# Kernel tuning notes

Measured on AMD Instinct MI355X. Metric: run time of the kernel, lower is better.

The kernel has to match this reference:

```python
import jax, jax.numpy as jnp
import numpy as np

B, N, D_IN, D, H_HEADS, DH, M_LAND, ITERS, NCLS = 2, 16384, 1024, 512, 8, 64, 256, 6, 2


def layer_norm(x, g, b, eps=1e-5):
    mu = x.mean(-1, keepdims=True)
    var = ((x - mu) ** 2).mean(-1, keepdims=True)
    return (x - mu) * jax.lax.rsqrt(var + eps) * g + b


def pinv_iter(x, iters):
    # Moore-Penrose pseudo-inverse via Newton-Schulz style iteration (lucidrains nystrom-attention)
    col = jnp.abs(x).sum(-1)
    row = jnp.abs(x).sum(-2)
    z = jnp.swapaxes(x, -1, -2) / (jnp.max(col) * jnp.max(row))
    I = jnp.eye(x.shape[-1], dtype=x.dtype)
    for _ in range(iters):
        xz = x @ z
        z = 0.25 * z @ (13.0 * I - xz @ (15.0 * I - xz @ (7.0 * I - xz)))
    return z


def depthwise_conv(x, w, pad_h, pad_w):
    # x: [B,C,H,W], w: [C,1,kh,kw], groups=C
    return jax.lax.conv_general_dilated(
        x, w, (1, 1), ((pad_h, pad_h), (pad_w, pad_w)),
        dimension_numbers=('NCHW', 'OIHW', 'NCHW'), feature_group_count=x.shape[1])


def nystrom_attention(x, w_qkv, w_out, b_out, res_w):
    b, n, _ = x.shape
    pad = (-n) % M_LAND
    xp = jnp.pad(x, ((0, 0), (pad, 0), (0, 0)))  # pad at front
    npad = n + pad
    qkv = xp @ w_qkv                              # [b, npad, 3D]
    q, k, v = jnp.split(qkv, 3, axis=-1)
    split_heads = lambda t: t.reshape(b, npad, H_HEADS, DH).transpose(0, 2, 1, 3)
    q = split_heads(q) * (DH ** -0.5)
    k = split_heads(k)
    v = split_heads(v)
    l = npad // M_LAND
    # landmarks: mean over contiguous groups '(m l) d -> m d'
    ql = q.reshape(b, H_HEADS, M_LAND, l, DH).mean(3)
    kl = k.reshape(b, H_HEADS, M_LAND, l, DH).mean(3)
    sim1 = jnp.einsum('bhnd,bhmd->bhnm', q, kl)   # [b,h,npad,m]
    sim2 = jnp.einsum('bhid,bhjd->bhij', ql, kl)  # [b,h,m,m]
    sim3 = jnp.einsum('bhmd,bhnd->bhmn', ql, k)   # [b,h,m,npad]
    a1 = jax.nn.softmax(sim1, -1)
    a2 = jax.nn.softmax(sim2, -1)
    a3 = jax.nn.softmax(sim3, -1)
    a2inv = pinv_iter(a2, ITERS)
    out = (a1 @ a2inv) @ (a3 @ v)                 # [b,h,npad,dh]
    # residual depthwise conv over sequence dim, kernel (33,1), per head
    out = out + depthwise_conv(v, res_w, 16, 0)
    out = out.transpose(0, 2, 1, 3).reshape(b, npad, D)
    out = out @ w_out + b_out                     # dropout is identity in eval
    return out[:, -n:]


def ppeg(x, Hs, Ws, w7, b7, w5, b5, w3, b3):
    Bx, _, C = x.shape
    cls_tok, feat = x[:, :1], x[:, 1:]
    f = feat.transpose(0, 2, 1).reshape(Bx, C, Hs, Ws)
    y = (f
         + depthwise_conv(f, w7, 3, 3) + b7[None, :, None, None]
         + depthwise_conv(f, w5, 2, 2) + b5[None, :, None, None]
         + depthwise_conv(f, w3, 1, 1) + b3[None, :, None, None])
    y = y.reshape(Bx, C, Hs * Ws).transpose(0, 2, 1)
    return jnp.concatenate([cls_tok, y], axis=1)


def _forward(x, w_feat, b_feat, cls_token, ln1_g, ln1_b, qkv1, out1_w, out1_b, res1_w,
             ppeg_w7, ppeg_b7, ppeg_w5, ppeg_b5, ppeg_w3, ppeg_b3,
             ln2_g, ln2_b, qkv2, out2_w, out2_b, res2_w, lnf_g, lnf_b, cls_w, cls_b):
    h = jax.nn.gelu(x @ w_feat + b_feat)          # feature embed (dropout off)
    n = h.shape[1]
    side = int(np.ceil(np.sqrt(n)))
    add = side * side - n
    h = jnp.concatenate([h, h[:, :add]], axis=1)  # pad bag to square
    cls = jnp.broadcast_to(cls_token, (h.shape[0], 1, D))
    h = jnp.concatenate([cls, h], axis=1)
    h = h + nystrom_attention(layer_norm(h, ln1_g, ln1_b), qkv1, out1_w, out1_b, res1_w)
    h = ppeg(h, side, side, ppeg_w7, ppeg_b7, ppeg_w5, ppeg_b5, ppeg_w3, ppeg_b3)
    h = h + nystrom_attention(layer_norm(h, ln2_g, ln2_b), qkv2, out2_w, out2_b, res2_w)
    feat0 = layer_norm(h, lnf_g, lnf_b)[:, 0]
    return feat0 @ cls_w + cls_b                  # logits [B, n_classes]


def setup_inputs() -> dict:
    key = jax.random.key(0)
    ks = jax.random.split(key, 16)
    s = jnp.float32(0.02)
    return {
        'x': jax.random.normal(ks[0], (B, N, D_IN), jnp.float32),
        'w_feat': jax.random.normal(ks[1], (D_IN, D), jnp.float32) * s,
        'b_feat': jnp.zeros((D,), jnp.float32),
        'cls_token': jax.random.normal(ks[2], (1, 1, D), jnp.float32) * jnp.float32(1e-6),
        'ln1_g': jnp.ones((D,), jnp.float32), 'ln1_b': jnp.zeros((D,), jnp.float32),
        'qkv1': jax.random.normal(ks[3], (D, 3 * D), jnp.float32) * s,
        'out1_w': jax.random.normal(ks[4], (D, D), jnp.float32) * s,
        'out1_b': jnp.zeros((D,), jnp.float32),
        'res1_w': jax.random.normal(ks[5], (H_HEADS, 1, 33, 1), jnp.float32) * s,
        'ppeg_w7': jax.random.normal(ks[6], (D, 1, 7, 7), jnp.float32) * s,
        'ppeg_b7': jnp.zeros((D,), jnp.float32),
        'ppeg_w5': jax.random.normal(ks[7], (D, 1, 5, 5), jnp.float32) * s,
        'ppeg_b5': jnp.zeros((D,), jnp.float32),
        'ppeg_w3': jax.random.normal(ks[8], (D, 1, 3, 3), jnp.float32) * s,
        'ppeg_b3': jnp.zeros((D,), jnp.float32),
        'ln2_g': jnp.ones((D,), jnp.float32), 'ln2_b': jnp.zeros((D,), jnp.float32),
        'qkv2': jax.random.normal(ks[9], (D, 3 * D), jnp.float32) * s,
        'out2_w': jax.random.normal(ks[10], (D, D), jnp.float32) * s,
        'out2_b': jnp.zeros((D,), jnp.float32),
        'res2_w': jax.random.normal(ks[11], (H_HEADS, 1, 33, 1), jnp.float32) * s,
        'lnf_g': jnp.ones((D,), jnp.float32), 'lnf_b': jnp.zeros((D,), jnp.float32),
        'cls_w': jax.random.normal(ks[12], (D, NCLS), jnp.float32) * s,
        'cls_b': jnp.zeros((NCLS,), jnp.float32),
    }


def reference(x, w_feat, b_feat, cls_token, ln1_g, ln1_b, qkv1, out1_w, out1_b, res1_w,
              ppeg_w7, ppeg_b7, ppeg_w5, ppeg_b5, ppeg_w3, ppeg_b3,
              ln2_g, ln2_b, qkv2, out2_w, out2_b, res2_w, lnf_g, lnf_b, cls_w, cls_b):
    return _forward(x, w_feat, b_feat, cls_token, ln1_g, ln1_b, qkv1, out1_w, out1_b, res1_w,
                    ppeg_w7, ppeg_b7, ppeg_w5, ppeg_b5, ppeg_w3, ppeg_b3,
                    ln2_g, ln2_b, qkv2, out2_w, out2_b, res2_w, lnf_g, lnf_b, cls_w, cls_b)
```

## Files before the change

kernel.cpp:

```cpp
#include <hip/hip_runtime.h>
#include <cstdint>
#include <cstddef>

#define BB 2
#define TT 16385
#define NPAD 16640
#define DD 512
#define HH 8
#define DHH 64
#define MLAND 256
#define PADF 255
#define A3KC 26
#define A3CH 640

typedef __attribute__((ext_vector_type(8))) _Float16 f16x8;
typedef __attribute__((ext_vector_type(4))) float f32x4;

__device__ __forceinline__ float gelu_f(float v) {
  float c = 0.7978845608028654f * (v + 0.044715f * v * v * v);
  return 0.5f * v * (1.0f + tanhf(c));
}

__device__ __forceinline__ unsigned short f16_1(float a) {
  _Float16 h = (_Float16)a;
  return __builtin_bit_cast(unsigned short, h);
}
__device__ __forceinline__ float f16f(unsigned u) {
  return (float)__builtin_bit_cast(_Float16, (unsigned short)(u & 0xffffu));
}
__device__ __forceinline__ unsigned pk_f16(float a, float b) {
  return (unsigned)f16_1(a) | ((unsigned)f16_1(b) << 16);
}
__device__ __forceinline__ void split2h(float a, float b, unsigned& hi, unsigned& lo) {
  _Float16 ah = (_Float16)a, bh = (_Float16)b;
  hi = (unsigned)__builtin_bit_cast(unsigned short, ah) |
       ((unsigned)__builtin_bit_cast(unsigned short, bh) << 16);
  lo = pk_f16(a - (float)ah, b - (float)bh);
}

__device__ __forceinline__ void gload16(const unsigned short* g, short* l) {
  __builtin_amdgcn_global_load_lds(
      (const __attribute__((address_space(1))) void*)g,
      (__attribute__((address_space(3))) void*)l, 16, 0, 0);
}

__global__ void k_set_cls(float* __restrict__ h, const float* __restrict__ cls) {
  h[(size_t)blockIdx.x * TT * DD + threadIdx.x] = cls[threadIdx.x];
}
__global__ void k_copy_cls(float* __restrict__ dst, const float* __restrict__ src) {
  size_t o = (size_t)blockIdx.x * TT * DD + threadIdx.x;
  dst[o] = src[o];
}

__global__ __launch_bounds__(256) void k_cvt_wt(
    const float* __restrict__ W, unsigned short* __restrict__ Wth, int K, int N) {
  __shared__ float tile[32][33];
  int kb = blockIdx.x * 32, nb = blockIdx.y * 32;
  int t = threadIdx.x;
  int tr = t >> 3, tc4 = (t & 7) * 4;
  float4 v = *(const float4*)(W + (size_t)(kb + tr) * N + nb + tc4);
  tile[tr][tc4 + 0] = v.x;
  tile[tr][tc4 + 1] = v.y;
  tile[tr][tc4 + 2] = v.z;
  tile[tr][tc4 + 3] = v.w;
  __syncthreads();
  int n = nb + tr;
  ushort4 hs;
  hs.x = f16_1(tile[tc4 + 0][tr]);
  hs.y = f16_1(tile[tc4 + 1][tr]);
  hs.z = f16_1(tile[tc4 + 2][tr]);
  hs.w = f16_1(tile[tc4 + 3][tr]);
  *(ushort4*)(Wth + (size_t)n * K + kb + tc4) = hs;
}

template <int MODE>
__global__ __launch_bounds__(512) void k_gemm_mfma(
    const float* __restrict__ A, const unsigned short* __restrict__ Aph,
    const unsigned short* __restrict__ Apl, const unsigned short* __restrict__ Wth,
    const float* __restrict__ bias, void* __restrict__ Cv, int M, int K, int N,
    int lda) {
  __shared__ short Ash[128][44];
  __shared__ short Asl[128][44];
  __shared__ short Bsh[256][44];
  const int t = threadIdx.x;
  int nRow = gridDim.x, nCol = gridDim.y;
  int lin = blockIdx.x + blockIdx.y * nRow;
  int chunk = 8 * nCol;
  int group = lin / chunk;
  int rem = lin - group * chunk;
  int gbase = group * 8;
  int Geff = nRow - gbase;
  if (Geff > 8) Geff = 8;
  const int rb = (gbase + rem % Geff) * 128;
  const int cb = (rem / Geff) * 256;
  const float* Ab = A;
  float* Cf = (float*)Cv;
  unsigned short* Ch = (unsigned short*)Cv;
  if (MODE == 2) {
    int b = blockIdx.z;
    Ab = A + (size_t)b * NPAD * DD + (size_t)PADF * DD;
    Cf = (float*)Cv + (size_t)b * TT * DD;
  }
  const int lane = t & 63, wv = t >> 6;
  const int wr = wv >> 2, wc = wv & 3;
  const int fr = lane & 15, kg = lane >> 4;
  const int srow = t >> 2, skh = (t & 3) * 8;
  const int brow = t >> 1, bkh = (t & 1) * 16;

  f32x4 acc[4][4];
  f32x4 zero4 = {0.f, 0.f, 0.f, 0.f};
#pragma unroll
  for (int i = 0; i < 4; ++i)
#pragma unroll
    for (int j = 0; j < 4; ++j) acc[i][j] = zero4;

  for (int k0 = 0; k0 < K; k0 += 32) {
    __syncthreads();
    if (MODE == 1) {
      const unsigned short* ph = Aph + (size_t)(rb + srow) * lda + k0 + skh;
      const unsigned short* pl = Apl + (size_t)(rb + srow) * lda + k0 + skh;
      *(uint4*)&Ash[srow][skh] = *(const uint4*)ph;
      *(uint4*)&Asl[srow][skh] = *(const uint4*)pl;
    } else {
      int grow = rb + srow;
      float4 f0 = {0, 0, 0, 0}, f1 = {0, 0, 0, 0};
      if (grow < M) {
        const float* p = Ab + (size_t)grow * lda + k0 + skh;
        f0 = *(const float4*)p;
        f1 = *(const float4*)(p + 4);
      }
      unsigned h0, h1, h2, h3, l0, l1, l2, l3;
      split2h(f0.x, f0.y, h0, l0);
      split2h(f0.z, f0.w, h1, l1);
      split2h(f1.x, f1.y, h2, l2);
      split2h(f1.z, f1.w, h3, l3);
      *(uint4*)&Ash[srow][skh] = make_uint4(h0, h1, h2, h3);
      *(uint4*)&Asl[srow][skh] = make_uint4(l0, l1, l2, l3);
    }
    {
      const unsigned short* ph = Wth + (size_t)(cb + brow) * K + k0 + bkh;
      *(uint4*)&Bsh[brow][bkh] = *(const uint4*)ph;
      *(uint4*)&Bsh[brow][bkh + 8] = *(const uint4*)(ph + 8);
    }
    __syncthreads();
    f16x8 ah[4], al[4];
#pragma unroll
    for (int mf = 0; mf < 4; ++mf) {
      ah[mf] = *(const f16x8*)&Ash[wr * 64 + mf * 16 + fr][kg * 8];
      al[mf] = *(const f16x8*)&Asl[wr * 64 + mf * 16 + fr][kg * 8];
    }
#pragma unroll
    for (int nf = 0; nf < 4; ++nf) {
      f16x8 bhf = *(const f16x8*)&Bsh[wc * 64 + nf * 16 + fr][kg * 8];
#pragma unroll
      for (int mf = 0; mf < 4; ++mf) {
        acc[mf][nf] =
            __builtin_amdgcn_mfma_f32_16x16x32_f16(ah[mf], bhf, acc[mf][nf], 0, 0, 0);
        acc[mf][nf] =
            __builtin_amdgcn_mfma_f32_16x16x32_f16(al[mf], bhf, acc[mf][nf], 0, 0, 0);
      }
    }
  }
#pragma unroll
  for (int mf = 0; mf < 4; ++mf) {
#pragma unroll
    for (int r = 0; r < 4; ++r) {
      int row = rb + wr * 64 + mf * 16 + kg * 4 + r;
      if (MODE == 2 && row >= M) continue;
      size_t orow = (MODE == 0) ? (size_t)(row + (row >> 14) + 1) : (size_t)row;
#pragma unroll
      for (int nf = 0; nf < 4; ++nf) {
        int col = cb + wc * 64 + nf * 16 + fr;
        float v = acc[mf][nf][r];
        if (MODE == 0) {
          Cf[orow * DD + col] = gelu_f(v + bias[col]);
        } else if (MODE == 1) {
          Ch[orow * (size_t)N + col] = f16_1(v);
        } else {
          float old = Cf[orow * DD + col];
          Cf[orow * DD + col] = old + v + bias[col];
        }
      }
    }
  }
}

__global__ __launch_bounds__(512) void k_gemm_qkv8(
    const unsigned short* __restrict__ Aph, const unsigned short* __restrict__ Wth,
    unsigned short* __restrict__ Ch) {
  __shared__ __align__(16) short Ah[2][128][32];
  __shared__ __align__(16) short Bs[2][256][32];
  const int t = threadIdx.x;
  int nRow = gridDim.x, nCol = gridDim.y;
  int lin = blockIdx.x + blockIdx.y * nRow;
  int chunk = 8 * nCol;
  int group = lin / chunk;
  int rem = lin - group * chunk;
  int gbase = group * 8;
  int Geff = nRow - gbase;
  if (Geff > 8) Geff = 8;
  const int rb = (gbase + rem % Geff) * 128;
  const int cb = (rem / Geff) * 256;
  const int lane = t & 63, wv = t >> 6;
  const int wr = wv >> 2, wc = wv & 3;
  const int fr = lane & 15, kg = lane >> 4;
  const int lr4 = lane >> 2;
  const int ss = (lane & 3) ^ (lr4 & 3);

  f32x4 acc[4][4];
  f32x4 zero4 = {0.f, 0.f, 0.f, 0.f};
#pragma unroll
  for (int i = 0; i < 4; ++i)
#pragma unroll
    for (int j = 0; j < 4; ++j) acc[i][j] = zero4;

  auto STAGE = [&](int kt, int bf) {
    const int k0 = kt * 32;
    {
      int lr = wv * 16;
      gload16(Aph + (size_t)(rb + lr + lr4) * DD + k0 + ss * 8, &Ah[bf][lr][0]);
    }
#pragma unroll
    for (int j = 0; j < 2; ++j) {
      int lr = wv * 32 + j * 16;
      gload16(Wth + (size_t)(cb + lr + lr4) * DD + k0 + ss * 8, &Bs[bf][lr][0]);
    }
  };

  STAGE(0, 0);
  STAGE(1, 1);
  const int sl = ((kg ^ (fr & 3))) * 8;
  for (int kt = 0; kt < 16; ++kt) {
    if (kt < 15) {
      asm volatile("s_waitcnt vmcnt(3)" ::: "memory");
    } else {
      asm volatile("s_waitcnt vmcnt(0)" ::: "memory");
    }
    __builtin_amdgcn_sched_barrier(0);
    __builtin_amdgcn_s_barrier();
    const int bf = kt & 1;
    f16x8 ah[4];
#pragma unroll
    for (int mf = 0; mf < 4; ++mf)
      ah[mf] = *(const f16x8*)&Ah[bf][wr * 64 + mf * 16 + fr][sl];
#pragma unroll
    for (int nf = 0; nf < 4; ++nf) {
      f16x8 bhf = *(const f16x8*)&Bs[bf][wc * 64 + nf * 16 + fr][sl];
#pragma unroll
      for (int mf = 0; mf < 4; ++mf)
        acc[mf][nf] =
            __builtin_amdgcn_mfma_f32_16x16x32_f16(ah[mf], bhf, acc[mf][nf], 0, 0, 0);
    }
    __builtin_amdgcn_s_barrier();
    if (kt + 2 < 16) STAGE(kt + 2, bf);
  }
#pragma unroll
  for (int mf = 0; mf < 4; ++mf) {
#pragma unroll
    for (int r = 0; r < 4; ++r) {
      int row = rb + wr * 64 + mf * 16 + kg * 4 + r;
#pragma unroll
      for (int nf = 0; nf < 4; ++nf) {
        int col = cb + wc * 64 + nf * 16 + fr;
        Ch[(size_t)row * 1536 + col] = f16_1(acc[mf][nf][r]);
      }
    }
  }
}

__global__ __launch_bounds__(512) void k_gemm_proj(
    const unsigned short* __restrict__ Af, const unsigned short* __restrict__ Wth,
    float* __restrict__ Cb, const float* __restrict__ bias) {
  __shared__ __align__(16) short Ah[2][128][32];
  __shared__ __align__(16) short Bs[2][256][32];
  const int t = threadIdx.x;
  int nRow = gridDim.x, nCol = gridDim.y;
  int lin = blockIdx.x + blockIdx.y * nRow;
  int chunk = 8 * nCol;
  int group = lin / chunk;
  int rem = lin - group * chunk;
  int gbase = group * 8;
  int Geff = nRow - gbase;
  if (Geff > 8) Geff = 8;
  const int rb = (gbase + rem % Geff) * 128;
  const int cb = (rem / Geff) * 256;
  const int lane = t & 63, wv = t >> 6;
  const int wr = wv >> 2, wc = wv & 3;
  const int fr = lane & 15, kg = lane >> 4;
  const int lr4 = lane >> 2;
  const int ss = (lane & 3) ^ (lr4 & 3);
  const size_t arow0 = (size_t)blockIdx.z * NPAD + PADF + rb;

  f32x4 acc[4][4];
  f32x4 zero4 = {0.f, 0.f, 0.f, 0.f};
#pragma unroll
  for (int i = 0; i < 4; ++i)
#pragma unroll
    for (int j = 0; j < 4; ++j) acc[i][j] = zero4;

  auto STAGE = [&](int kt, int bf) {
    const int k0 = kt * 32;
    {
      int lr = wv * 16;
      gload16(Af + (arow0 + lr + lr4) * DD + k0 + ss * 8, &Ah[bf][lr][0]);
    }
#pragma unroll
    for (int j = 0; j < 2; ++j) {
      int lr = wv * 32 + j * 16;
      gload16(Wth + (size_t)(cb + lr + lr4) * DD + k0 + ss * 8, &Bs[bf][lr][0]);
    }
  };

  STAGE(0, 0);
  STAGE(1, 1);
  const int sl = ((kg ^ (fr & 3))) * 8;
  for (int kt = 0; kt < 16; ++kt) {
    if (kt < 15) {
      asm volatile("s_waitcnt vmcnt(3)" ::: "memory");
    } else {
      asm volatile("s_waitcnt vmcnt(0)" ::: "memory");
    }
    __builtin_amdgcn_sched_barrier(0);
    __builtin_amdgcn_s_barrier();
    const int bf = kt & 1;
    f16x8 ah[4];
#pragma unroll
    for (int mf = 0; mf < 4; ++mf)
      ah[mf] = *(const f16x8*)&Ah[bf][wr * 64 + mf * 16 + fr][sl];
#pragma unroll
    for (int nf = 0; nf < 4; ++nf) {
      f16x8 bhf = *(const f16x8*)&Bs[bf][wc * 64 + nf * 16 + fr][sl];
#pragma unroll
      for (int mf = 0; mf < 4; ++mf)
        acc[mf][nf] =
            __builtin_amdgcn_mfma_f32_16x16x32_f16(ah[mf], bhf, acc[mf][nf], 0, 0, 0);
    }
    __builtin_amdgcn_s_barrier();
    if (kt + 2 < 16) STAGE(kt + 2, bf);
  }
  float* Cf = Cb + (size_t)blockIdx.z * TT * DD;
#pragma unroll
  for (int mf = 0; mf < 4; ++mf) {
#pragma unroll
    for (int r = 0; r < 4; ++r) {
      int row = rb + wr * 64 + mf * 16 + kg * 4 + r;
      if (row >= TT) continue;
#pragma unroll
      for (int nf = 0; nf < 4; ++nf) {
        int col = cb + wc * 64 + nf * 16 + fr;
        float old = Cf[(size_t)row * DD + col];
        Cf[(size_t)row * DD + col] = old + acc[mf][nf][r] + bias[col];
      }
    }
  }
}

__global__ __launch_bounds__(256) void k_ln_pad(
    unsigned short* __restrict__ xph, const float* __restrict__ h,
    const float* __restrict__ gam, const float* __restrict__ bet) {
  int w = threadIdx.x >> 6, lane = threadIdx.x & 63;
  int row = blockIdx.x * 4 + w;
  if (row >= BB * TT) return;
  int b = row / TT, i = row - b * TT;
  const float* src = h + (size_t)row * DD;
  float4 x0 = *(const float4*)(src + lane * 4);
  float4 x1 = *(const float4*)(src + 256 + lane * 4);
  float s = x0.x + x0.y + x0.z + x0.w + x1.x + x1.y + x1.z + x1.w;
  for (int o = 32; o; o >>= 1) s += __shfl_xor(s, o);
  float mu = s * (1.f / 512.f);
  float q = (x0.x - mu) * (x0.x - mu) + (x0.y - mu) * (x0.y - mu) +
            (x0.z - mu) * (x0.z - mu) + (x0.w - mu) * (x0.w - mu) +
            (x1.x - mu) * (x1.x - mu) + (x1.y - mu) * (x1.y - mu) +
            (x1.z - mu) * (x1.z - mu) + (x1.w - mu) * (x1.w - mu);
  for (int o = 32; o; o >>= 1) q += __shfl_xor(q, o);
  float rs = rsqrtf(q * (1.f / 512.f) + 1e-5f);
  float4 g0 = *(const float4*)(gam + lane * 4);
  float4 g1 = *(const float4*)(gam + 256 + lane * 4);
  float4 b0 = *(const float4*)(bet + lane * 4);
  float4 b1 = *(const float4*)(bet + 256 + lane * 4);
  float4 o0, o1;
  o0.x = (x0.x - mu) * rs * g0.x + b0.x;
  o0.y = (x0.y - mu) * rs * g0.y + b0.y;
  o0.z = (x0.z - mu) * rs * g0.z + b0.z;
  o0.w = (x0.w - mu) * rs * g0.w + b0.w;
  o1.x = (x1.x - mu) * rs * g1.x + b1.x;
  o1.y = (x1.y - mu) * rs * g1.y + b1.y;
  o1.z = (x1.z - mu) * rs * g1.z + b1.z;
  o1.w = (x1.w - mu) * rs * g1.w + b1.w;
  size_t ro = ((size_t)b * NPAD + PADF + i) * DD;
  *(uint2*)(xph + ro + lane * 4) = make_uint2(pk_f16(o0.x, o0.y), pk_f16(o0.z, o0.w));
  *(uint2*)(xph + ro + 256 + lane * 4) =
      make_uint2(pk_f16(o1.x, o1.y), pk_f16(o1.z, o1.w));
}

__global__ void k_zero_pad(unsigned short* __restrict__ xph) {
  int r = blockIdx.x;
  int b = r / PADF, j = r - b * PADF;
  size_t ro = ((size_t)b * NPAD + j) * DD;
  ((unsigned*)(xph + ro))[threadIdx.x] = 0u;
}

__global__ __launch_bounds__(256) void k_landmarks(
    float* __restrict__ ql, float* __restrict__ kl,
    const unsigned short* __restrict__ qkv) {
  int t = threadIdx.x;
  int mi = t >> 6, d = t & 63;
  int blk = blockIdx.x;
  int bh = blk >> 6, mg = blk & 63;
  int b = bh >> 3, h = bh & 7;
  int m = mg * 4 + mi;
  const unsigned short* base = qkv + (size_t)b * NPAD * 1536 + h * 64 + d;
  float sq = 0.f, sk = 0.f;
  int t0 = m * 65;
  for (int j = 0; j < 65; ++j) {
    const unsigned short* p = base + (size_t)(t0 + j) * 1536;
    sq += f16f(p[0]);
    sk += f16f(p[512]);
  }
  ql[((size_t)bh * 256 + m) * 64 + d] = sq * (0.125f / 65.f);
  kl[((size_t)bh * 256 + m) * 64 + d] = sk * (1.f / 65.f);
}

__global__ __launch_bounds__(256) void k_sim2(
    float* __restrict__ sim, const float* __restrict__ ql, const float* __restrict__ kl) {
  __shared__ __align__(16) float Aq[64][68];
  __shared__ __align__(16) float Bk[64][68];
  int t = threadIdx.x;
  int tj = blockIdx.x, ti = blockIdx.y, bh = blockIdx.z;
  int r = t >> 2, cc = (t & 3) * 16;
  const float* ap = ql + ((size_t)bh * 256 + ti * 64 + r) * 64 + cc;
  const float* bp = kl + ((size_t)bh * 256 + tj * 64 + r) * 64 + cc;
#pragma unroll
  for (int i = 0; i < 16; i += 4) {
    *(float4*)&Aq[r][cc + i] = *(const float4*)(ap + i);
    *(float4*)&Bk[r][cc + i] = *(const float4*)(bp + i);
  }
  __syncthreads();
  int tx = t & 15, ty = t >> 4;
  float acc[4][4];
#pragma unroll
  for (int i = 0; i < 4; ++i)
#pragma unroll
    for (int j = 0; j < 4; ++j) acc[i][j] = 0.f;
  for (int d = 0; d < 64; d += 4) {
    float4 a4[4], b4[4];
#pragma unroll
    for (int ii = 0; ii < 4; ++ii) a4[ii] = *(float4*)&Aq[ty * 4 + ii][d];
#pragma unroll
    for (int jj = 0; jj < 4; ++jj) b4[jj] = *(float4*)&Bk[tx * 4 + jj][d];
#pragma unroll
    for (int ii = 0; ii < 4; ++ii)
#pragma unroll
      for (int jj = 0; jj < 4; ++jj)
        acc[ii][jj] += a4[ii].x * b4[jj].x + a4[ii].y * b4[jj].y + a4[ii].z * b4[jj].z +
                       a4[ii].w * b4[jj].w;
  }
#pragma unroll
  for (int ii = 0; ii < 4; ++ii)
#pragma unroll
    for (int jj = 0; jj < 4; ++jj)
      sim[((size_t)bh * 256 + ti * 64 + ty * 4 + ii) * 256 + tj * 64 + tx * 4 + jj] =
          acc[ii][jj];
}

__global__ __launch_bounds__(256) void k_softmax256(float* __restrict__ a) {
  int w = threadIdx.x >> 6, lane = threadIdx.x & 63;
  size_t row = (size_t)blockIdx.x * 4 + w;
  float* p = a + row * 256 + lane * 4;
  float4 v = *(float4*)p;
  float m = fmaxf(fmaxf(v.x, v.y), fmaxf(v.z, v.w));
  for (int o = 32; o; o >>= 1) m = fmaxf(m, __shfl_xor(m, o));
  v.x = expf(v.x - m); v.y = expf(v.y - m);
  v.z = expf(v.z - m); v.w = expf(v.w - m);
  float s = v.x + v.y + v.z + v.w;
  for (int o = 32; o; o >>= 1) s += __shfl_xor(s, o);
  float inv = 1.f / s;
  v.x *= inv; v.y *= inv; v.z *= inv; v.w *= inv;
  *(float4*)p = v;
}

__global__ void k_pinv_sums(float* __restrict__ red, const float* __restrict__ a2) {
  int bh = blockIdx.x, t = threadIdx.x;
  const float* Ab = a2 + (size_t)bh * 65536;
  float s = 0.f;
// ... 419 lines not shown
#pragma unroll
    for (int kw = 0; kw < 2; ++kw) {
      f16x8 vf[4], pf[4];
#pragma unroll
      for (int mf = 0; mf < 4; ++mf)
        vf[mf] = *(const f16x8*)&W2t[mf * 16 + fr][kw * 32 + kg * 8];
#pragma unroll
      for (int nf = 0; nf < 4; ++nf)
        pf[nf] = *(const f16x8*)&Ps[w][nf * 16 + fr][kw * 32 + kg * 8];
#pragma unroll
      for (int mf = 0; mf < 4; ++mf)
#pragma unroll
        for (int nf = 0; nf < 4; ++nf)
          oacc[mf][nf] = __builtin_amdgcn_mfma_f32_16x16x32_f16(vf[mf], pf[nf],
                                                                oacc[mf][nf], 0, 0, 0);
    }
  }
#pragma unroll
  for (int nf = 0; nf < 4; ++nf) {
    Lp[nf] += __shfl_xor(Lp[nf], 16);
    Lp[nf] += __shfl_xor(Lp[nf], 32);
  }
#pragma unroll
  for (int nf = 0; nf < 4; ++nf) {
    float inv = 1.0f / Lp[nf];
    int tok = n0 + w * 64 + nf * 16 + fr;
#pragma unroll
    for (int mf = 0; mf < 4; ++mf) {
      f32x4 o = oacc[mf][nf];
      ushort4 hs;
      hs.x = f16_1(o[0] * inv);
      hs.y = f16_1(o[1] * inv);
      hs.z = f16_1(o[2] * inv);
      hs.w = f16_1(o[3] * inv);
      *(ushort4*)(attf + ((size_t)b * NPAD + tok) * DD + h * 64 + mf * 16 + kg * 4) = hs;
    }
  }
}

__global__ __launch_bounds__(256) void k_convres(
    unsigned short* __restrict__ attf, const unsigned short* __restrict__ qkv,
    const float* __restrict__ resw) {
  __shared__ float vS[96][68];
  __shared__ float w33[33];
  int t = threadIdx.x;
  int tb = blockIdx.x, bh = blockIdx.y;
  int b = bh >> 3, h = bh & 7;
  int n0 = tb * 64;
  if (t < 33) w33[t] = resw[h * 33 + t];
  int sc = (t & 3) * 16;
#pragma unroll
  for (int pass = 0; pass < 2; ++pass) {
    int r = (t >> 2) + pass * 64;
    if (r < 96) {
      int seq = n0 - 16 + r;
      if (seq >= 0 && seq < NPAD) {
        const unsigned short* p =
            qkv + ((size_t)b * NPAD + seq) * 1536 + 1024 + h * 64 + sc;
        uint4 u0 = *(const uint4*)p;
        uint4 u1 = *(const uint4*)(p + 8);
        float4 f0 = make_float4(f16f(u0.x), f16f(u0.x >> 16), f16f(u0.y),
                                f16f(u0.y >> 16));
        float4 f1 = make_float4(f16f(u0.z), f16f(u0.z >> 16), f16f(u0.w),
                                f16f(u0.w >> 16));
        float4 f2 = make_float4(f16f(u1.x), f16f(u1.x >> 16), f16f(u1.y),
                                f16f(u1.y >> 16));
        float4 f3 = make_float4(f16f(u1.z), f16f(u1.z >> 16), f16f(u1.w),
                                f16f(u1.w >> 16));
        *(float4*)&vS[r][sc + 0] = f0;
        *(float4*)&vS[r][sc + 4] = f1;
        *(float4*)&vS[r][sc + 8] = f2;
        *(float4*)&vS[r][sc + 12] = f3;
      } else {
        float4 z = make_float4(0.f, 0.f, 0.f, 0.f);
        *(float4*)&vS[r][sc + 0] = z;
        *(float4*)&vS[r][sc + 4] = z;
        *(float4*)&vS[r][sc + 8] = z;
        *(float4*)&vS[r][sc + 12] = z;
      }
    }
  }
  __syncthreads();
  int tg = t >> 5;
  int d2 = (t & 31) * 2;
  float ax[8], ay[8];
#pragma unroll
  for (int j = 0; j < 8; ++j) { ax[j] = 0.f; ay[j] = 0.f; }
#pragma unroll
  for (int rr = 0; rr < 40; ++rr) {
    float2 v = *(float2*)&vS[tg * 8 + rr][d2];
#pragma unroll
    for (int j = 0; j < 8; ++j) {
      int k = rr - j;
      if (k >= 0 && k < 33) {
        ax[j] += w33[k] * v.x;
        ay[j] += w33[k] * v.y;
      }
    }
  }
#pragma unroll
  for (int j = 0; j < 8; ++j) {
    size_t off = ((size_t)b * NPAD + n0 + tg * 8 + j) * DD + h * 64 + d2;
    unsigned u = *(unsigned*)(attf + off);
    float x0 = f16f(u) + ax[j];
    float x1 = f16f(u >> 16) + ay[j];
    *(unsigned*)(attf + off) = pk_f16(x0, x1);
  }
}

__global__ __launch_bounds__(128) void k_ppeg(
    float* __restrict__ hB, const float* __restrict__ hA,
    const float* __restrict__ w7, const float* __restrict__ b7,
    const float* __restrict__ w5, const float* __restrict__ b5,
    const float* __restrict__ w3, const float* __restrict__ b3) {
  __shared__ float cw[49][128];
  int t = threadIdx.x;
  int i = blockIdx.x >> 2;
  int j0 = (blockIdx.x & 3) * 32;
  int cg = blockIdx.y, b = blockIdx.z;
  int c = cg * 128 + t;
#pragma unroll
  for (int k = 0; k < 49; ++k) cw[k][t] = w7[c * 49 + k];
#pragma unroll
  for (int di = 0; di < 5; ++di)
#pragma unroll
    for (int dj = 0; dj < 5; ++dj)
      cw[(di + 1) * 7 + dj + 1][t] += w5[c * 25 + di * 5 + dj];
#pragma unroll
  for (int di = 0; di < 3; ++di)
#pragma unroll
    for (int dj = 0; dj < 3; ++dj)
      cw[(di + 2) * 7 + dj + 2][t] += w3[c * 9 + di * 3 + dj];
  cw[24][t] += 1.0f;
  float bias = b7[c] + b5[c] + b3[c];
  const float* base = hA + (size_t)b * TT * DD + DD + c;
  float* obase = hB + (size_t)b * TT * DD + DD + c;
  float acc[32];
#pragma unroll
  for (int j = 0; j < 32; ++j) acc[j] = bias;
  for (int di = 0; di < 7; ++di) {
    int ii = i + di - 3;
    if ((unsigned)ii >= 128u) continue;
    float win[38];
#pragma unroll
    for (int w = 0; w < 38; ++w) {
      int col = j0 - 3 + w;
      win[w] = ((unsigned)col < 128u) ? base[(size_t)(ii * 128 + col) * DD] : 0.f;
    }
#pragma unroll
    for (int dj = 0; dj < 7; ++dj) {
      float wv = cw[di * 7 + dj][t];
#pragma unroll
      for (int j = 0; j < 32; ++j) acc[j] += win[j + dj] * wv;
    }
  }
#pragma unroll
  for (int j = 0; j < 32; ++j) obase[(size_t)(i * 128 + j0 + j) * DD] = acc[j];
}

__global__ __launch_bounds__(512) void k_final(
    float* __restrict__ out, const float* __restrict__ h,
    const float* __restrict__ g, const float* __restrict__ be,
    const float* __restrict__ cw, const float* __restrict__ cbias) {
  __shared__ float sm[16];
  int t = threadIdx.x;
  for (int b = 0; b < 2; ++b) {
    const float* row = h + (size_t)b * TT * DD;
    float x = row[t];
    float s = x;
    for (int o = 32; o; o >>= 1) s += __shfl_xor(s, o);
    if ((t & 63) == 0) sm[t >> 6] = s;
    __syncthreads();
    float mu = 0.f;
    for (int i = 0; i < 8; ++i) mu += sm[i];
    mu *= (1.f / 512.f);
    __syncthreads();
    float d = x - mu;
    s = d * d;
    for (int o = 32; o; o >>= 1) s += __shfl_xor(s, o);
    if ((t & 63) == 0) sm[t >> 6] = s;
    __syncthreads();
    float var = 0.f;
    for (int i = 0; i < 8; ++i) var += sm[i];
    var *= (1.f / 512.f);
    float rs = rsqrtf(var + 1e-5f);
    __syncthreads();
    float f = d * rs * g[t] + be[t];
    float p0 = f * cw[2 * t], p1 = f * cw[2 * t + 1];
    for (int o = 32; o; o >>= 1) {
      p0 += __shfl_xor(p0, o);
      p1 += __shfl_xor(p1, o);
    }
    if ((t & 63) == 0) {
      sm[t >> 6] = p0;
      sm[8 + (t >> 6)] = p1;
    }
    __syncthreads();
    if (t == 0) {
      float q0 = 0.f, q1 = 0.f;
      for (int i = 0; i < 8; ++i) {
        q0 += sm[i];
        q1 += sm[8 + i];
      }
      out[b * 2 + 0] = q0 + cbias[0];
      out[b * 2 + 1] = q1 + cbias[1];
    }
    __syncthreads();
  }
}

static void run_attn(float* h, const float* lng, const float* lnb,
                     const float* wqkv, const float* wout, const float* bout,
                     const float* resw, float* xp, unsigned short* qkvh, float* ql,
                     float* kl, float* a2, float* z0, float* z1, float* xz, float* xz2,
                     float* yB, float* yC, float* bv, float* w2, float* red,
                     float* Sbuf, unsigned short* wth, hipStream_t stream) {
  unsigned short* xph = (unsigned short*)xp;
  k_zero_pad<<<BB * PADF, 256, 0, stream>>>(xph);
  k_ln_pad<<<(BB * TT + 3) / 4, 256, 0, stream>>>(xph, h, lng, lnb);
  k_cvt_wt<<<dim3(DD / 32, 1536 / 32), 256, 0, stream>>>(wqkv, wth, DD, 1536);
  k_gemm_qkv8<<<dim3(BB * NPAD / 128, 1536 / 256), 512, 0, stream>>>(xph, wth, qkvh);
  k_landmarks<<<1024, 256, 0, stream>>>(ql, kl, qkvh);
  float* pacc = Sbuf;
  float* pL = Sbuf + (size_t)A3KC * 4096 * 64;
  k_a3v_mfma<<<dim3(16, A3KC), 256, 0, stream>>>(pacc, pL, ql, qkvh);
  k_a3v_red<<<4096, 64, 0, stream>>>(bv, pacc, pL);
  k_sim2<<<dim3(4, 4, 16), 256, 0, stream>>>(a2, ql, kl);
  k_softmax256<<<1024, 256, 0, stream>>>(a2);
  k_pinv_sums<<<16, 256, 0, stream>>>(red, a2);
  k_pinv_scale<<<1, 256, 0, stream>>>(red);
  k_zinit<<<dim3(256, 16), 256, 0, stream>>>(z0, a2, red);
  float* zc = z0;
  float* zn = z1;
  float* P = xz;
  float* Pn = xz2;
  k_bmm_poly<<<dim3(4, 4, 16), 256, 0, stream>>>(a2, zc, nullptr, P, 1.f, 0.f, 0.f, 256);
  for (int it = 0; it < 6; ++it) {
    k_bmm_poly<<<dim3(4, 4, 16), 256, 0, stream>>>(P, P, P, yB, 1.f, 15.f, -7.f, 256);
    k_bmm_poly<<<dim3(4, 4, 16), 256, 0, stream>>>(P, yB, nullptr, yC, -1.f, 13.f, 0.f, 256);
    k_bmm_dual<<<dim3(4, 4, 32), 256, 0, stream>>>(zc, P, yC, zn, Pn, 0.25f);
    float* tmp = zc; zc = zn; zn = tmp;
    tmp = P; P = Pn; Pn = tmp;
  }
  k_bmm_poly<<<dim3(1, 4, 16), 256, 0, stream>>>(zc, bv, nullptr, w2, 1.f, 0.f, 0.f, 64);
  k_att1<<<dim3(NPAD / 256, 16), 256, 0, stream>>>(xph, qkvh, kl, w2);
  k_convres<<<dim3(NPAD / 64, 16), 256, 0, stream>>>(xph, qkvh, resw);
  k_cvt_wt<<<dim3(DD / 32, DD / 32), 256, 0, stream>>>(wout, wth, DD, DD);
  k_gemm_proj<<<dim3(129, 2, BB), 512, 0, stream>>>(xph, wth, h, bout);
}

extern "C" void kernel_launch(void* const* d_in, const int* in_sizes, int n_in,
                              void* d_out, int out_size, void* d_ws, size_t ws_size,
                              hipStream_t stream) {
  const float* x        = (const float*)d_in[0];
  const float* w_feat   = (const float*)d_in[1];
  const float* b_feat   = (const float*)d_in[2];
  const float* cls_tok  = (const float*)d_in[3];
  const float* ln1_g    = (const float*)d_in[4];
  const float* ln1_b    = (const float*)d_in[5];
  const float* qkv1     = (const float*)d_in[6];
  const float* out1_w   = (const float*)d_in[7];
  const float* out1_b   = (const float*)d_in[8];
  const float* res1_w   = (const float*)d_in[9];
  const float* ppeg_w7  = (const float*)d_in[10];
  const float* ppeg_b7  = (const float*)d_in[11];
  const float* ppeg_w5  = (const float*)d_in[12];
  const float* ppeg_b5  = (const float*)d_in[13];
  const float* ppeg_w3  = (const float*)d_in[14];
  const float* ppeg_b3  = (const float*)d_in[15];
  const float* ln2_g    = (const float*)d_in[16];
  const float* ln2_b    = (const float*)d_in[17];
  const float* qkv2     = (const float*)d_in[18];
  const float* out2_w   = (const float*)d_in[19];
  const float* out2_b   = (const float*)d_in[20];
  const float* res2_w   = (const float*)d_in[21];
  const float* lnf_g    = (const float*)d_in[22];
  const float* lnf_b    = (const float*)d_in[23];
  const float* cls_w    = (const float*)d_in[24];
  const float* cls_b    = (const float*)d_in[25];

  float* ws = (float*)d_ws;
  size_t off = 0;
  float* hA  = ws + off; off += (size_t)BB * TT * DD;
  float* hB  = ws + off; off += (size_t)BB * TT * DD;
  float* xp  = ws + off; off += (size_t)BB * NPAD * DD;
  float* qkvf = ws + off; off += (size_t)BB * NPAD * 3 * DD;
  unsigned short* qkvh = (unsigned short*)qkvf;
  float* ql  = ws + off; off += (size_t)BB * HH * 256 * 64;
  float* kl  = ws + off; off += (size_t)BB * HH * 256 * 64;
  float* a2  = ws + off; off += (size_t)16 * 65536;
  float* z0  = ws + off; off += (size_t)16 * 65536;
  float* z1  = ws + off; off += (size_t)16 * 65536;
  float* xz  = ws + off; off += (size_t)16 * 65536;
  float* xz2 = ws + off; off += (size_t)16 * 65536;
  float* yB  = ws + off; off += (size_t)16 * 65536;
  float* yC  = ws + off; off += (size_t)16 * 65536;
  float* bv  = ws + off; off += (size_t)BB * HH * 256 * 64;
  float* w2  = ws + off; off += (size_t)BB * HH * 256 * 64;
  float* red = ws + off; off += 8448;
  unsigned short* wth = (unsigned short*)(ws + off); off += 393216;

  k_set_cls<<<2, 512, 0, stream>>>(hA, cls_tok);
  k_cvt_wt<<<dim3(1024 / 32, DD / 32), 256, 0, stream>>>(w_feat, wth, 1024, DD);
  k_gemm_mfma<0><<<dim3(32768 / 128, DD / 256), 512, 0, stream>>>(
      x, nullptr, nullptr, wth, b_feat, hA, 32768, 1024, DD, 1024);
  run_attn(hA, ln1_g, ln1_b, qkv1, out1_w, out1_b, res1_w, xp, qkvh, ql, kl, a2, z0, z1,
           xz, xz2, yB, yC, bv, w2, red, hB, wth, stream);
  k_copy_cls<<<2, 512, 0, stream>>>(hB, hA);
  k_ppeg<<<dim3(512, 4, 2), 128, 0, stream>>>(hB, hA, ppeg_w7, ppeg_b7, ppeg_w5, ppeg_b5,
                                              ppeg_w3, ppeg_b3);
  run_attn(hB, ln2_g, ln2_b, qkv2, out2_w, out2_b, res2_w, xp, qkvh, ql, kl, a2, z0, z1,
           xz, xz2, yB, yC, bv, w2, red, hA, wth, stream);
  k_final<<<1, 512, 0, stream>>>((float*)d_out, hB, lnf_g, lnf_b, cls_w, cls_b);
}
```

Before: 1.374 ms.

## Rewrite feature GEMM with fp16 input, async LDS loads and double buffering

A separate kernel now converts the fp32 input x to fp16 into the qkv workspace. The feature-projection GEMM then uses the single fp16 operand instead of the split hi/lo pair, which halves the MFMA count. A/B tiles are streamed with global_load_lds into swizzled, double-buffered shared memory, with explicit vmcnt waits and barriers. The cost is an extra conversion pass over x and the lost low-order compensation term, which lowers feature precision.

```diff
diff --git a/kernel.cpp b/kernel.cpp
--- a/kernel.cpp
+++ b/kernel.cpp
@@ -50,6 +50,19 @@
 __global__ void k_copy_cls(float* __restrict__ dst, const float* __restrict__ src) {
   size_t o = (size_t)blockIdx.x * TT * DD + threadIdx.x;
   dst[o] = src[o];
+}
+
+__global__ __launch_bounds__(256) void k_cvt_x(
+    unsigned short* __restrict__ xh, const float* __restrict__ x) {
+  size_t i = ((size_t)blockIdx.x * 256 + threadIdx.x) * 8;
+  float4 a = *(const float4*)(x + i);
+  float4 b = *(const float4*)(x + i + 4);
+  uint4 u;
+  u.x = pk_f16(a.x, a.y);
+  u.y = pk_f16(a.z, a.w);
+  u.z = pk_f16(b.x, b.y);
+  u.w = pk_f16(b.z, b.w);
+  *(uint4*)(xh + i) = u;
 }
 
 __global__ __launch_bounds__(256) void k_cvt_wt(
@@ -73,15 +86,11 @@
   *(ushort4*)(Wth + (size_t)n * K + kb + tc4) = hs;
 }
 
-template <int MODE>
-__global__ __launch_bounds__(512) void k_gemm_mfma(
-    const float* __restrict__ A, const unsigned short* __restrict__ Aph,
-    const unsigned short* __restrict__ Apl, const unsigned short* __restrict__ Wth,
-    const float* __restrict__ bias, void* __restrict__ Cv, int M, int K, int N,
-    int lda) {
-  __shared__ short Ash[128][44];
-  __shared__ short Asl[128][44];
-  __shared__ short Bsh[256][44];
+__global__ __launch_bounds__(512) void k_gemm_feat(
+    const unsigned short* __restrict__ Xh, const unsigned short* __restrict__ Wth,
+    float* __restrict__ Cf, const float* __restrict__ bias) {
+  __shared__ __align__(16) short Ah[2][128][32];
+  __shared__ __align__(16) short Bs[2][256][32];
   const int t = threadIdx.x;
   int nRow = gridDim.x, nCol = gridDim.y;
   int lin = blockIdx.x + blockIdx.y * nRow;
@@ -93,19 +102,11 @@
   if (Geff > 8) Geff = 8;
   const int rb = (gbase + rem % Geff) * 128;
   const int cb = (rem / Geff) * 256;
-  const float* Ab = A;
-  float* Cf = (float*)Cv;
-  unsigned short* Ch = (unsigned short*)Cv;
-  if (MODE == 2) {
-    int b = blockIdx.z;
-    Ab = A + (size_t)b * NPAD * DD + (size_t)PADF * DD;
-    Cf = (float*)Cv + (size_t)b * TT * DD;
-  }
   const int lane = t & 63, wv = t >> 6;
   const int wr = wv >> 2, wc = wv & 3;
   const int fr = lane & 15, kg = lane >> 4;
-  const int srow = t >> 2, skh = (t & 3) * 8;
-  const int brow = t >> 1, bkh = (t & 1) * 16;
+  const int lr4 = lane >> 2;
+  const int ss = (lane & 3) ^ (lr4 & 3);
 
   f32x4 acc[4][4];
   f32x4 zero4 = {0.f, 0.f, 0.f, 0.f};
@@ -114,72 +115,56 @@
 #pragma unroll
     for (int j = 0; j < 4; ++j) acc[i][j] = zero4;
 
-  for (int k0 = 0; k0 < K; k0 += 32) {
-    __syncthreads();
-    if (MODE == 1) {
-      const unsigned short* ph = Aph + (size_t)(rb + srow) * lda + k0 + skh;
-      const unsigned short* pl = Apl + (size_t)(rb + srow) * lda + k0 + skh;
-      *(uint4*)&Ash[srow][skh] = *(const uint4*)ph;
-      *(uint4*)&Asl[srow][skh] = *(const uint4*)pl;
+  auto STAGE = [&](int kt, int bf) {
+    const int k0 = kt * 32;
+    {
+      int lr = wv * 16;
+      gload16(Xh + (size_t)(rb + lr + lr4) * 1024 + k0 + ss * 8, &Ah[bf][lr][0]);
+    }
+#pragma unroll
+    for (int j = 0; j < 2; ++j) {
+      int lr = wv * 32 + j * 16;
+      gload16(Wth + (size_t)(cb + lr + lr4) * 1024 + k0 + ss * 8, &Bs[bf][lr][0]);
+    }
+  };
+
+  STAGE(0, 0);
+  STAGE(1, 1);
+  const int sl = ((kg ^ (fr & 3))) * 8;
+  for (int kt = 0; kt < 32; ++kt) {
+    if (kt < 31) {
+      asm volatile("s_waitcnt vmcnt(3)" ::: "memory");
     } else {
-      int grow = rb + srow;
-      float4 f0 = {0, 0, 0, 0}, f1 = {0, 0, 0, 0};
-      if (grow < M) {
-        const float* p = Ab + (size_t)grow * lda + k0 + skh;
-        f0 = *(const float4*)p;
-        f1 = *(const float4*)(p + 4);
-      }
-      unsigned h0, h1, h2, h3, l0, l1, l2, l3;
-      split2h(f0.x, f0.y, h0, l0);
-      split2h(f0.z, f0.w, h1, l1);
-      split2h(f1.x, f1.y, h2, l2);
-      split2h(f1.z, f1.w, h3, l3);
-      *(uint4*)&Ash[srow][skh] = make_uint4(h0, h1, h2, h3);
-      *(uint4*)&Asl[srow][skh] = make_uint4(l0, l1, l2, l3);
-    }
-    {
-      const unsigned short* ph = Wth + (size_t)(cb + brow) * K + k0 + bkh;
-      *(uint4*)&Bsh[brow][bkh] = *(const uint4*)ph;
-      *(uint4*)&Bsh[brow][bkh + 8] = *(const uint4*)(ph + 8);
-    }
-    __syncthreads();
-    f16x8 ah[4], al[4];
-#pragma unroll
-    for (int mf = 0; mf < 4; ++mf) {
-      ah[mf] = *(const f16x8*)&Ash[wr * 64 + mf * 16 + fr][kg * 8];
-      al[mf] = *(const f16x8*)&Asl[wr * 64 + mf * 16 + fr][kg * 8];
-    }
+      asm volatile("s_waitcnt vmcnt(0)" ::: "memory");
+    }
+    __builtin_amdgcn_sched_barrier(0);
+    __builtin_amdgcn_s_barrier();
+    const int bf = kt & 1;
+    f16x8 ah[4];
+#pragma unroll
+    for (int mf = 0; mf < 4; ++mf)
+      ah[mf] = *(const f16x8*)&Ah[bf][wr * 64 + mf * 16 + fr][sl];
 #pragma unroll
     for (int nf = 0; nf < 4; ++nf) {
-      f16x8 bhf = *(const f16x8*)&Bsh[wc * 64 + nf * 16 + fr][kg * 8];
-#pragma unroll
-      for (int mf = 0; mf < 4; ++mf) {
+      f16x8 bhf = *(const f16x8*)&Bs[bf][wc * 64 + nf * 16 + fr][sl];
+#pragma unroll
+      for (int mf = 0; mf < 4; ++mf)
         acc[mf][nf] =
             __builtin_amdgcn_mfma_f32_16x16x32_f16(ah[mf], bhf, acc[mf][nf], 0, 0, 0);
-        acc[mf][nf] =
-            __builtin_amdgcn_mfma_f32_16x16x32_f16(al[mf], bhf, acc[mf][nf], 0, 0, 0);
-      }
-    }
+    }
+    __builtin_amdgcn_s_barrier();
+    if (kt + 2 < 32) STAGE(kt + 2, bf);
   }
 #pragma unroll
   for (int mf = 0; mf < 4; ++mf) {
 #pragma unroll
     for (int r = 0; r < 4; ++r) {
       int row = rb + wr * 64 + mf * 16 + kg * 4 + r;
-      if (MODE == 2 && row >= M) continue;
-      size_t orow = (MODE == 0) ? (size_t)(row + (row >> 14) + 1) : (size_t)row;
+      size_t orow = (size_t)(row + (row >> 14) + 1);
 #pragma unroll
       for (int nf = 0; nf < 4; ++nf) {
         int col = cb + wc * 64 + nf * 16 + fr;
-        float v = acc[mf][nf][r];
-        if (MODE == 0) {
-          Cf[orow * DD + col] = gelu_f(v + bias[col]);
-        } else if (MODE == 1) {
-          Ch[orow * (size_t)N + col] = f16_1(v);
-        } else {
-          float old = Cf[orow * DD + col];
-          Cf[orow * DD + col] = old + v + bias[col];
-        }
+        Cf[orow * DD + col] = gelu_f(acc[mf][nf][r] + bias[col]);
       }
     }
   }
@@ -1205,8 +1190,8 @@
 
   k_set_cls<<<2, 512, 0, stream>>>(hA, cls_tok);
   k_cvt_wt<<<dim3(1024 / 32, DD / 32), 256, 0, stream>>>(w_feat, wth, 1024, DD);
-  k_gemm_mfma<0><<<dim3(32768 / 128, DD / 256), 512, 0, stream>>>(
-      x, nullptr, nullptr, wth, b_feat, hA, 32768, 1024, DD, 1024);
+  k_cvt_x<<<16384, 256, 0, stream>>>(qkvh, x);
+  k_gemm_feat<<<dim3(256, 2), 512, 0, stream>>>(qkvh, wth, hA, b_feat);
   run_attn(hA, ln1_g, ln1_b, qkv1, out1_w, out1_b, res1_w, xp, qkvh, ql, kl, a2, z0, z1,
            xz, xz2, yB, yC, bv, w2, red, hB, wth, stream);
   k_copy_cls<<<2, 512, 0, stream>>>(hB, hA);
```

Measured after the change: 1.359 ms. No clear change (-1.1%).
